# Kernel optimization log

Hardware: AMD Instinct MI355X
Metric: run time of the kernel (lower is better)

## Reference

```python
import jax, jax.numpy as jnp
import numpy as np

D_MODEL = 1024
N_HEAD = 16
HEAD_DIM = D_MODEL // N_HEAD
ROPE_BASE = 10000.0


def _weight_quant(w):
    # BitNet b1.58 ternary weight quant with per-tensor absmean scale (STE).
    scale = jnp.clip(jnp.mean(jnp.abs(w)), 1e-5, None)
    wq = jnp.clip(jnp.round(w / scale), -1.0, 1.0) * scale
    return w + jax.lax.stop_gradient(wq - w)


def _act_quant(x):
    # Per-token int8 absmax activation quant (STE).
    scale = 127.0 / jnp.clip(jnp.max(jnp.abs(x), axis=-1, keepdims=True), 1e-5, None)
    xq = jnp.clip(jnp.round(x * scale), -128.0, 127.0) / scale
    return x + jax.lax.stop_gradient(xq - x)


def _bitlinear(x, w):
    # y = act_quant(x) @ weight_quant(w).T   (torch Linear convention, no bias)
    return _act_quant(x) @ _weight_quant(w).T


def _rope(x, pos):
    # x: [B, H, T, D]; half-split rotation.
    d = x.shape[-1]
    inv_freq = 1.0 / (ROPE_BASE ** (jnp.arange(0, d, 2, dtype=jnp.float32) / d))
    ang = pos[:, None].astype(jnp.float32) * inv_freq[None, :]  # [T, D/2]
    cos, sin = jnp.cos(ang), jnp.sin(ang)
    x1, x2 = x[..., : d // 2], x[..., d // 2 :]
    return jnp.concatenate([x1 * cos - x2 * sin, x1 * sin + x2 * cos], axis=-1)


def setup_inputs() -> dict:
    key = jax.random.key(0)
    k0, k1, k2, k3, k4 = jax.random.split(key, 5)
    B, T = 2, 2048
    s = 1.0 / np.sqrt(D_MODEL)
    return {
        "x": jax.random.normal(k0, (B, T, D_MODEL), dtype=jnp.float32),
        "Wq": jax.random.normal(k1, (D_MODEL, D_MODEL), dtype=jnp.float32) * s,
        "Wk": jax.random.normal(k2, (D_MODEL, D_MODEL), dtype=jnp.float32) * s,
        "Wv": jax.random.normal(k3, (D_MODEL, D_MODEL), dtype=jnp.float32) * s,
        "Wo": jax.random.normal(k4, (D_MODEL, D_MODEL), dtype=jnp.float32) * s,
    }


def reference(x, Wq, Wk, Wv, Wo):
    B, T, C = x.shape
    pos = jnp.arange(T)
    def heads(y):
        return y.reshape(B, T, N_HEAD, HEAD_DIM).transpose(0, 2, 1, 3)  # [B,H,T,D]
    q = _rope(heads(_bitlinear(x, Wq)), pos)
    k = _rope(heads(_bitlinear(x, Wk)), pos)
    v = heads(_bitlinear(x, Wv))
    scores = jnp.einsum("bhqd,bhkd->bhqk", q, k) / jnp.sqrt(jnp.float32(HEAD_DIM))
    causal = jnp.tril(jnp.ones((T, T), dtype=bool))
    scores = jnp.where(causal[None, None], scores, jnp.finfo(scores.dtype).min)
    att = jax.nn.softmax(scores, axis=-1)
    y = jnp.einsum("bhqk,bhkd->bhqd", att, v)  # [B,H,T,D]
    y = y.transpose(0, 2, 1, 3).reshape(B, T, C)
    return _bitlinear(y, Wo)
```

## Files before the change

kernel.cpp:

```cpp
#include <hip/hip_runtime.h>
#include <hip/hip_bf16.h>
#include <math.h>

typedef __bf16 bf16_t;
typedef signed char i8_t;
typedef __attribute__((ext_vector_type(8))) __bf16 bf16x8;
typedef __attribute__((ext_vector_type(4))) __bf16 bf16x4;
typedef __attribute__((ext_vector_type(4))) float f32x4;
typedef __attribute__((ext_vector_type(4))) int i32x4;

typedef __attribute__((address_space(3))) void lds_void_t;
typedef const __attribute__((address_space(1))) void glb_void_t;
#define GLOAD_LDS(g, l) __builtin_amdgcn_global_load_lds((glb_void_t*)(g), (lds_void_t*)(l), 16, 0, 0)

#define MFMA16(a,b,c) __builtin_amdgcn_mfma_f32_16x16x32_bf16(a,b,c,0,0,0)
#define MFMAI8(a,b,c) __builtin_amdgcn_mfma_i32_16x16x64_i8(a,b,c,0,0,0)

#if __has_builtin(__builtin_amdgcn_exp2f)
#define EXP2F(x) __builtin_amdgcn_exp2f(x)
#else
#define EXP2F(x) exp2f(x)
#endif

static constexpr int TSEQ = 2048;
static constexpr int CDIM = 1024;
#define NEG_BIG (-1.0e30f)
#define Q_PRESCALE 0.18033688011112042f
#define ROPE_C 0.41524101190971284f

__global__ __launch_bounds__(256) void wreduce(const float* __restrict__ W0, const float* __restrict__ W1,
                                               const float* __restrict__ W2, const float* __restrict__ W3,
                                               double* __restrict__ partial) {
  int w = blockIdx.x >> 6, b = blockIdx.x & 63;
  const float* W = (w==0)?W0:(w==1)?W1:(w==2)?W2:W3;
  const float* base = W + (size_t)b * 16384;
  double s = 0.0;
  for (int i = threadIdx.x * 4; i < 16384; i += 1024) {
    float4 v = *(const float4*)(base + i);
    s += (double)fabsf(v.x) + (double)fabsf(v.y) + (double)fabsf(v.z) + (double)fabsf(v.w);
  }
  #pragma unroll
  for (int off = 1; off < 64; off <<= 1) s += __shfl_xor(s, off);
  __shared__ double red[4];
  if ((threadIdx.x & 63) == 0) red[threadIdx.x >> 6] = s;
  __syncthreads();
  if (threadIdx.x == 0) partial[blockIdx.x] = red[0] + red[1] + red[2] + red[3];
}

__global__ __launch_bounds__(256) void prep(const float* __restrict__ W0, const float* __restrict__ W1,
                                            const float* __restrict__ W2, const float* __restrict__ W3,
                                            const double* __restrict__ partial, float* __restrict__ wscale,
                                            i8_t* __restrict__ wq_all,
                                            const float* __restrict__ xg, i8_t* __restrict__ xqg,
                                            float* __restrict__ rowfac, float2* __restrict__ ropetab) {
  int bid = blockIdx.x;
  if (bid < 4096) {
    int w = bid >> 10;
    double ssum = 0.0;
    for (int i = 0; i < 64; ++i) ssum += partial[w * 64 + i];
    float s = fmaxf((float)(ssum * (1.0 / 1048576.0)), 1e-5f);
    if ((bid & 1023) == 0 && threadIdx.x == 0) wscale[w] = s;
    const float* W = (w==0)?W0:(w==1)?W1:(w==2)?W2:W3;
    int off = ((bid & 1023) * 256 + threadIdx.x) * 4;
    float4 v = *(const float4*)(W + off);
    char4 q;
    q.x = (i8_t)(int)fminf(fmaxf(rintf(v.x / s), -1.f), 1.f);
    q.y = (i8_t)(int)fminf(fmaxf(rintf(v.y / s), -1.f), 1.f);
    q.z = (i8_t)(int)fminf(fmaxf(rintf(v.z / s), -1.f), 1.f);
    q.w = (i8_t)(int)fminf(fmaxf(rintf(v.w / s), -1.f), 1.f);
    *(char4*)(wq_all + (size_t)w * 1048576 + off) = q;
  } else if (bid < 8192) {
    int r = bid - 4096;
    float4 v = *(const float4*)(xg + (size_t)r * 1024 + threadIdx.x * 4);
    float mx = fmaxf(fmaxf(fabsf(v.x), fabsf(v.y)), fmaxf(fabsf(v.z), fabsf(v.w)));
    #pragma unroll
    for (int off = 1; off < 64; off <<= 1) mx = fmaxf(mx, __shfl_xor(mx, off));
    __shared__ float red[4];
    if ((threadIdx.x & 63) == 0) red[threadIdx.x >> 6] = mx;
    __syncthreads();
    mx = fmaxf(fmaxf(red[0], red[1]), fmaxf(red[2], red[3]));
    mx = fmaxf(mx, 1e-5f);
    float scale = 127.0f / mx;
    if (threadIdx.x == 0) rowfac[r] = mx * (1.0f / 127.0f);
    char4 q;
    q.x = (i8_t)(int)fminf(fmaxf(rintf(v.x * scale), -128.f), 127.f);
    q.y = (i8_t)(int)fminf(fmaxf(rintf(v.y * scale), -128.f), 127.f);
    q.z = (i8_t)(int)fminf(fmaxf(rintf(v.z * scale), -128.f), 127.f);
    q.w = (i8_t)(int)fminf(fmaxf(rintf(v.w * scale), -128.f), 127.f);
    *(char4*)(xqg + (size_t)r * 1024 + threadIdx.x * 4) = q;
  } else {
    int t = (bid - 8192) * 8 + (threadIdx.x >> 5);
    int ii = threadIdx.x & 31;
    float ang = (float)t * exp2f(-(float)ii * ROPE_C);
    float sn, cs;
    sincosf(ang, &sn, &cs);
    ropetab[t * 32 + ii] = make_float2(cs, sn);
  }
}

__global__ __launch_bounds__(256) void actquant(const float* __restrict__ xg, i8_t* __restrict__ xqg,
                                                float* __restrict__ rowfac) {
  int r = blockIdx.x;
  float4 v = *(const float4*)(xg + (size_t)r * 1024 + threadIdx.x * 4);
  float mx = fmaxf(fmaxf(fabsf(v.x), fabsf(v.y)), fmaxf(fabsf(v.z), fabsf(v.w)));
  #pragma unroll
  for (int off = 1; off < 64; off <<= 1) mx = fmaxf(mx, __shfl_xor(mx, off));
  __shared__ float red[4];
  if ((threadIdx.x & 63) == 0) red[threadIdx.x >> 6] = mx;
  __syncthreads();
  mx = fmaxf(fmaxf(red[0], red[1]), fmaxf(red[2], red[3]));
  mx = fmaxf(mx, 1e-5f);
  float scale = 127.0f / mx;
  if (threadIdx.x == 0) rowfac[r] = mx * (1.0f / 127.0f);
  char4 q;
  q.x = (i8_t)(int)fminf(fmaxf(rintf(v.x * scale), -128.f), 127.f);
  q.y = (i8_t)(int)fminf(fmaxf(rintf(v.y * scale), -128.f), 127.f);
  q.z = (i8_t)(int)fminf(fmaxf(rintf(v.z * scale), -128.f), 127.f);
  q.w = (i8_t)(int)fminf(fmaxf(rintf(v.w * scale), -128.f), 127.f);
  *(char4*)(xqg + (size_t)r * 1024 + threadIdx.x * 4) = q;
}

__global__ __launch_bounds__(256) void gemm_qkv(const i8_t* __restrict__ xq, const i8_t* __restrict__ wq_all,
                                                const float* __restrict__ wscale, const float* __restrict__ rowfac,
                                                const float2* __restrict__ ropetab,
                                                bf16_t* __restrict__ qb, bf16_t* __restrict__ kb,
                                                bf16_t* __restrict__ vtb) {
  const int z = blockIdx.z;
  const i8_t* Bw = wq_all + (size_t)z * 1048576;
  const int m0 = blockIdx.x * 128, n0 = blockIdx.y * 128;
  const int tid = threadIdx.x;
  const int wave = tid >> 6, lane = tid & 63, quad = lane >> 4, l16 = lane & 15;
  const int wm = wave >> 1, wn = wave & 1;
  __shared__ __align__(16) i8_t As[128 * 64];
  __shared__ __align__(16) i8_t Bs[128 * 64];
  i32x4 zero = {0, 0, 0, 0};
  i32x4 acc[4][4];
  #pragma unroll
  for (int i = 0; i < 4; ++i)
    #pragma unroll
    for (int j = 0; j < 4; ++j) acc[i][j] = zero;

  const int row_s = tid >> 2;
  const int cg16 = (((tid & 3) - (row_s >> 1)) & 3) * 16;
  const int sw16 = ((quad + (l16 >> 1)) & 3) * 16;

  for (int kt = 0; kt < 16; ++kt) {
    __syncthreads();
    #pragma unroll
    for (int v2 = 0; v2 < 2; ++v2) {
      int v = tid + v2 * 256;
      int row = row_s + v2 * 64;
      GLOAD_LDS(&xq[(size_t)(m0 + row) * 1024 + kt * 64 + cg16], &As[v * 16]);
      GLOAD_LDS(&Bw[(size_t)(n0 + row) * 1024 + kt * 64 + cg16], &Bs[v * 16]);
    }
    __syncthreads();
    i32x4 af[4], bfr[4];
    #pragma unroll
    for (int i = 0; i < 4; ++i) af[i] = *(const i32x4*)&As[(wm * 64 + i * 16 + l16) * 64 + sw16];
    #pragma unroll
    for (int j = 0; j < 4; ++j) bfr[j] = *(const i32x4*)&Bs[(wn * 64 + j * 16 + l16) * 64 + sw16];
    if (z == 2) {
      #pragma unroll
      for (int i = 0; i < 4; ++i)
        #pragma unroll
        for (int j = 0; j < 4; ++j) acc[i][j] = MFMAI8(bfr[i], af[j], acc[i][j]);
    } else {
      #pragma unroll
      for (int i = 0; i < 4; ++i)
        #pragma unroll
        for (int j = 0; j < 4; ++j) acc[i][j] = MFMAI8(af[i], bfr[j], acc[i][j]);
    }
  }
  float ws = wscale[z] * (z == 0 ? Q_PRESCALE : 1.0f);
  if (z <= 1) {
    bf16_t* dst = (z == 0) ? qb : kb;
    const int h = (n0 >> 6) + wn;
    #pragma unroll
    for (int i = 0; i < 4; ++i) {
      #pragma unroll
      for (int r = 0; r < 4; ++r) {
        int m = m0 + wm * 64 + i * 16 + quad * 4 + r;
        float rf = rowfac[m] * ws;
        int b = m >> 11, t = m & 2047;
        bf16_t* drow = dst + (((size_t)b * 16 + h) * 2048 + t) * 64;
        #pragma unroll
        for (int j = 0; j < 2; ++j) {
          int dd1 = j * 16 + l16;
          float2 cs2 = ropetab[t * 32 + dd1];
          float v1 = (float)acc[i][j][r] * rf;
          float v2 = (float)acc[i][j + 2][r] * rf;
          drow[dd1]      = (bf16_t)(v1 * cs2.x - v2 * cs2.y);
          drow[dd1 + 32] = (bf16_t)(v1 * cs2.y + v2 * cs2.x);
        }
      }
    }
  } else {
    const int b = m0 >> 11;
    const int tbase = (m0 & 2047) + wm * 64;
    float rfj[4];
    #pragma unroll
    for (int j = 0; j < 4; ++j) rfj[j] = rowfac[m0 + wm * 64 + j * 16 + l16] * ws;
    #pragma unroll
    for (int i = 0; i < 4; ++i) {
      #pragma unroll
      for (int r = 0; r < 4; ++r) {
        int nrow = n0 + wn * 64 + i * 16 + quad * 4 + r;
        int h = nrow >> 6, dd = nrow & 63;
        bf16_t* vrow = vtb + (((size_t)b * 16 + h) * 64 + dd) * 2048 + tbase;
        #pragma unroll
        for (int j = 0; j < 4; ++j) vrow[j * 16 + l16] = (bf16_t)((float)acc[i][j][r] * rfj[j]);
      }
    }
  }
}

__global__ __launch_bounds__(256) void gemm_out(const i8_t* __restrict__ yq, const i8_t* __restrict__ wo,
                                                const float* __restrict__ wscale, const float* __restrict__ rowfac,
                                                float* __restrict__ out) {
  const int m0 = blockIdx.x * 128, n0 = blockIdx.y * 128;
  const int tid = threadIdx.x;
  const int wave = tid >> 6, lane = tid & 63, quad = lane >> 4, l16 = lane & 15;
  const int wm = wave >> 1, wn = wave & 1;
  __shared__ __align__(16) i8_t As[128 * 64];
  __shared__ __align__(16) i8_t Bs[128 * 64];
  i32x4 zero = {0, 0, 0, 0};
  i32x4 acc[4][4];
  #pragma unroll
  for (int i = 0; i < 4; ++i)
    #pragma unroll
    for (int j = 0; j < 4; ++j) acc[i][j] = zero;

  const int row_s = tid >> 2;
  const int cg16 = (((tid & 3) - (row_s >> 1)) & 3) * 16;
  const int sw16 = ((quad + (l16 >> 1)) & 3) * 16;

  for (int kt = 0; kt < 16; ++kt) {
    __syncthreads();
    #pragma unroll
    for (int v2 = 0; v2 < 2; ++v2) {
      int v = tid + v2 * 256;
      int row = row_s + v2 * 64;
      GLOAD_LDS(&yq[(size_t)(m0 + row) * 1024 + kt * 64 + cg16], &As[v * 16]);
      GLOAD_LDS(&wo[(size_t)(n0 + row) * 1024 + kt * 64 + cg16], &Bs[v * 16]);
    }
    __syncthreads();
    i32x4 af[4], bfr[4];
    #pragma unroll
    for (int i = 0; i < 4; ++i) af[i] = *(const i32x4*)&As[(wm * 64 + i * 16 + l16) * 64 + sw16];
    #pragma unroll
    for (int j = 0; j < 4; ++j) bfr[j] = *(const i32x4*)&Bs[(wn * 64 + j * 16 + l16) * 64 + sw16];
    #pragma unroll
    for (int i = 0; i < 4; ++i)
      #pragma unroll
      for (int j = 0; j < 4; ++j) acc[i][j] = MFMAI8(af[i], bfr[j], acc[i][j]);
  }
  float ws = wscale[3];
  #pragma unroll
  for (int i = 0; i < 4; ++i) {
    #pragma unroll
    for (int r = 0; r < 4; ++r) {
      int m = m0 + wm * 64 + i * 16 + quad * 4 + r;
      float rf = rowfac[m] * ws;
      #pragma unroll
      for (int j = 0; j < 4; ++j) {
        int n = n0 + wn * 64 + j * 16 + l16;
        out[(size_t)m * 1024 + n] = (float)acc[i][j][r] * rf;
      }
    }
  }
}

__global__ __launch_bounds__(512) void flash_attn(const bf16_t* __restrict__ qg, const bf16_t* __restrict__ kg,
                                                  const bf16_t* __restrict__ vtg, float* __restrict__ yf) {
  const int lid = (int)blockIdx.y * 8 + (int)blockIdx.x;
  const int p  = (lid >> 3) & 7;
  const int bh = (lid & 7) * 4 + (lid >> 6);
  const int tid = threadIdx.x;
  const int wave = tid >> 6, lane = tid & 63;
  const int quad = lane >> 4, l16 = lane & 15;

  __shared__ __align__(16) bf16_t Kb[2][64 * 64];
  __shared__ __align__(16) bf16_t Vb[2][64 * 64];
  __shared__ __align__(16) bf16_t Pl[8][16 * 72];

  const int b = bh >> 4, h = bh & 15;
  bf16_t* Pw = &Pl[wave][0];

  const int r0 = tid >> 3, cblk = tid & 7;
  const int ldsOff0 = r0 * 64 + ((cblk ^ (r0 & 7)) * 8);
  const size_t bhbase = (size_t)bh * 131072;
  const bf16_t* kbase0 = kg + bhbase + r0 * 64 + cblk * 8;
  const bf16_t* vbase0 = vtg + bhbase + r0 * 2048 + cblk * 8;

  int kf_off[4][2];
  #pragma unroll
  for (int n = 0; n < 4; ++n)
    #pragma unroll
    for (int c = 0; c < 2; ++c)
      kf_off[n][c] = (n * 16 + l16) * 64 + (((c * 4 + quad) ^ (l16 & 7)) * 8);

  bf16x8 ones;
  #pragma unroll
  for (int j = 0; j < 8; ++j) ones[j] = (bf16_t)1.0f;
  f32x4 zero = {0.f, 0.f, 0.f, 0.f};

  bf16x8 kpre = *(const bf16x8*)(kbase0);
  bf16x8 vpre = *(const bf16x8*)(vbase0);

  int cum = 0;
  #pragma unroll 1
  for (int tsel = 0; tsel < 2; ++tsel) {
    const int qt = tsel ? (15 - p) : p;
    const int kcmax = 2 * qt + 1;
    const int qbw = qt * 128 + wave * 16;

    const bf16_t* qrowp = qg + ((size_t)bh * TSEQ + qbw + l16) * 64;
    bf16x8 aq0 = *(const bf16x8*)(qrowp + quad * 8);
    bf16x8 aq1 = *(const bf16x8*)(qrowp + 32 + quad * 8);

    f32x4 o[4], o5;
    #pragma unroll
    for (int i = 0; i < 4; ++i) o[i] = zero;
    o5 = zero;

    #pragma unroll 1
    for (int kc = 0; kc <= kcmax; ++kc, ++cum) {
      const int buf = cum & 1;
      bf16_t* Kt = &Kb[buf][0];
      bf16_t* Vt = &Vb[buf][0];
      *(bf16x8*)&Kt[ldsOff0] = kpre;
      *(bf16x8*)&Vt[ldsOff0] = vpre;
      __syncthreads();
      int nkc = (kc < kcmax) ? (kc + 1) : ((tsel == 0) ? 0 : -1);
      if (nkc >= 0) {
        kpre = *(const bf16x8*)(kbase0 + nkc * 4096);
        vpre = *(const bf16x8*)(vbase0 + nkc * 64);
      }

      f32x4 s[4];
      #pragma unroll
      for (int n = 0; n < 4; ++n) {
        bf16x8 bk0 = *(const bf16x8*)&Kt[kf_off[n][0]];
        bf16x8 bk1 = *(const bf16x8*)&Kt[kf_off[n][1]];
        s[n] = MFMA16(aq1, bk1, MFMA16(aq0, bk0, zero));
      }
      if (kc * 64 + 63 > qbw) {
        #pragma unroll
        for (int n = 0; n < 4; ++n)
          #pragma unroll
          for (int r = 0; r < 4; ++r) {
            int kpos = kc * 64 + n * 16 + l16;
            int qpos = qbw + quad * 4 + r;
            if (kpos > qpos) s[n][r] = NEG_BIG;
          }
      }
      #pragma unroll
      for (int n = 0; n < 4; ++n)
        #pragma unroll
        for (int r = 0; r < 4; ++r)
          Pw[(quad * 4 + r) * 72 + n * 16 + l16] = (bf16_t)EXP2F(s[n][r]);

      bf16x8 ap0 = *(const bf16x8*)&Pw[l16 * 72 + quad * 8];
      bf16x8 ap1 = *(const bf16x8*)&Pw[l16 * 72 + 32 + quad * 8];
      #pragma unroll
      for (int nh = 0; nh < 4; ++nh) {
        bf16x8 bv0 = *(const bf16x8*)&Vt[kf_off[nh][0]];
        bf16x8 bv1 = *(const bf16x8*)&Vt[kf_off[nh][1]];
        o[nh] = MFMA16(ap1, bv1, MFMA16(ap0, bv0, o[nh]));
      }
      o5 = MFMA16(ap1, ones, MFMA16(ap0, ones, o5));
    }

    #pragma unroll
    for (int r = 0; r < 4; ++r) {
      float invl = 1.0f / o5[r];
      int t = qbw + quad * 4 + r;
      float* yrow = yf + ((size_t)b * TSEQ + t) * CDIM + h * 64;
      #pragma unroll
      for (int nh = 0; nh < 4; ++nh) yrow[nh * 16 + l16] = o[nh][r] * invl;
    }
  }
}

extern "C" void kernel_launch(void* const* d_in, const int* in_sizes, int n_in,
                              void* d_out, int out_size, void* d_ws, size_t ws_size,
                              hipStream_t stream) {
  const float* x  = (const float*)d_in[0];
  const float* Wq = (const float*)d_in[1];
  const float* Wk = (const float*)d_in[2];
  const float* Wv = (const float*)d_in[3];
  const float* Wo = (const float*)d_in[4];
  float* out = (float*)d_out;

  char* ws = (char*)d_ws;
  double* wpartial = (double*)(ws);
  float* wscale   = (float*)(ws + 4096);
  float* rowfacx  = (float*)(ws + 8192);
  float* rowfacy  = (float*)(ws + 8192 + 16384);
  i8_t* wq_all    = (i8_t*)(ws + 65536);
  i8_t* xq        = wq_all + 4194304;
  bf16_t* qb      = (bf16_t*)(xq + 4194304);
  bf16_t* kb      = qb + 4194304;
  bf16_t* vtb     = kb + 4194304;
  float*  yf      = (float*)(vtb + 4194304);
  float2* ropetab = (float2*)(yf + 4194304);
  i8_t* yq        = xq;

  wreduce<<<256, 256, 0, stream>>>(Wq, Wk, Wv, Wo, wpartial);
  prep<<<8448, 256, 0, stream>>>(Wq, Wk, Wv, Wo, wpartial, wscale, wq_all, x, xq, rowfacx, ropetab);
  gemm_qkv<<<dim3(32, 8, 3), 256, 0, stream>>>(xq, wq_all, wscale, rowfacx, ropetab, qb, kb, vtb);
  flash_attn<<<dim3(8, 32), 512, 0, stream>>>(qb, kb, vtb, yf);
  actquant<<<4096, 256, 0, stream>>>(yf, yq, rowfacy);
  gemm_out<<<dim3(32, 8), 256, 0, stream>>>(yq, wq_all + 3 * 1048576, wscale, rowfacy, out);
}
```

Measured before the change: 171.9 us.

## Halve flash-attention query tile to 64 rows with 4 waves and 512 blocks

Changes the flash attention work split from 128-query tiles handled by 8 waves to 64-query tiles handled by 4 waves, doubling the grid to 512 blocks while keeping the paired causal tile scheduling (p and 31-p). Each thread now loads two 16-byte chunks of K and V per 64-key tile, because there are half as many threads. The aim is more blocks for better CU occupancy and finer causal load balance on the MI355X. In exchange, each K/V tile is reused by fewer query rows, so global K/V traffic roughly doubles.

After: 181.8 us. +5.7%, slower.

```diff
diff --git a/kernel.cpp b/kernel.cpp
--- a/kernel.cpp
+++ b/kernel.cpp
@@ -270,27 +270,31 @@
   }
 }
 
-__global__ __launch_bounds__(512) void flash_attn(const bf16_t* __restrict__ qg, const bf16_t* __restrict__ kg,
+__global__ __launch_bounds__(256) void flash_attn(const bf16_t* __restrict__ qg, const bf16_t* __restrict__ kg,
                                                   const bf16_t* __restrict__ vtg, float* __restrict__ yf) {
   const int lid = (int)blockIdx.y * 8 + (int)blockIdx.x;
-  const int p  = (lid >> 3) & 7;
-  const int bh = (lid & 7) * 4 + (lid >> 6);
+  const int p  = (lid >> 3) & 15;
+  const int bh = (lid & 7) * 4 + (lid >> 7);
   const int tid = threadIdx.x;
   const int wave = tid >> 6, lane = tid & 63;
   const int quad = lane >> 4, l16 = lane & 15;
 
   __shared__ __align__(16) bf16_t Kb[2][64 * 64];
   __shared__ __align__(16) bf16_t Vb[2][64 * 64];
-  __shared__ __align__(16) bf16_t Pl[8][16 * 72];
+  __shared__ __align__(16) bf16_t Pl[4][16 * 72];
 
   const int b = bh >> 4, h = bh & 15;
   bf16_t* Pw = &Pl[wave][0];
 
   const int r0 = tid >> 3, cblk = tid & 7;
-  const int ldsOff0 = r0 * 64 + ((cblk ^ (r0 & 7)) * 8);
+  const int swz8 = ((cblk ^ (r0 & 7)) * 8);
+  const int ldsOffA = r0 * 64 + swz8;
+  const int ldsOffB = ldsOffA + 32 * 64;
   const size_t bhbase = (size_t)bh * 131072;
-  const bf16_t* kbase0 = kg + bhbase + r0 * 64 + cblk * 8;
-  const bf16_t* vbase0 = vtg + bhbase + r0 * 2048 + cblk * 8;
+  const bf16_t* kbaseA = kg + bhbase + r0 * 64 + cblk * 8;
+  const bf16_t* kbaseB = kbaseA + 32 * 64;
+  const bf16_t* vbaseA = vtg + bhbase + r0 * 2048 + cblk * 8;
+  const bf16_t* vbaseB = vbaseA + 32 * 2048;
 
   int kf_off[4][2];
   #pragma unroll
@@ -304,15 +308,17 @@
   for (int j = 0; j < 8; ++j) ones[j] = (bf16_t)1.0f;
   f32x4 zero = {0.f, 0.f, 0.f, 0.f};
 
-  bf16x8 kpre = *(const bf16x8*)(kbase0);
-  bf16x8 vpre = *(const bf16x8*)(vbase0);
+  bf16x8 kpreA = *(const bf16x8*)(kbaseA);
+  bf16x8 kpreB = *(const bf16x8*)(kbaseB);
+  bf16x8 vpreA = *(const bf16x8*)(vbaseA);
+  bf16x8 vpreB = *(const bf16x8*)(vbaseB);
 
   int cum = 0;
   #pragma unroll 1
   for (int tsel = 0; tsel < 2; ++tsel) {
-    const int qt = tsel ? (15 - p) : p;
-    const int kcmax = 2 * qt + 1;
-    const int qbw = qt * 128 + wave * 16;
+    const int qt = tsel ? (31 - p) : p;
+    const int kcmax = qt;
+    const int qbw = qt * 64 + wave * 16;
 
     const bf16_t* qrowp = qg + ((size_t)bh * TSEQ + qbw + l16) * 64;
     bf16x8 aq0 = *(const bf16x8*)(qrowp + quad * 8);
@@ -328,13 +334,17 @@
       const int buf = cum & 1;
       bf16_t* Kt = &Kb[buf][0];
       bf16_t* Vt = &Vb[buf][0];
-      *(bf16x8*)&Kt[ldsOff0] = kpre;
-      *(bf16x8*)&Vt[ldsOff0] = vpre;
+      *(bf16x8*)&Kt[ldsOffA] = kpreA;
+      *(bf16x8*)&Kt[ldsOffB] = kpreB;
+      *(bf16x8*)&Vt[ldsOffA] = vpreA;
+      *(bf16x8*)&Vt[ldsOffB] = vpreB;
       __syncthreads();
       int nkc = (kc < kcmax) ? (kc + 1) : ((tsel == 0) ? 0 : -1);
       if (nkc >= 0) {
-        kpre = *(const bf16x8*)(kbase0 + nkc * 4096);
-        vpre = *(const bf16x8*)(vbase0 + nkc * 64);
+        kpreA = *(const bf16x8*)(kbaseA + nkc * 4096);
+        kpreB = *(const bf16x8*)(kbaseB + nkc * 4096);
+        vpreA = *(const bf16x8*)(vbaseA + nkc * 64);
+        vpreB = *(const bf16x8*)(vbaseB + nkc * 64);
       }
 
       f32x4 s[4];
@@ -409,7 +419,7 @@
   wreduce<<<256, 256, 0, stream>>>(Wq, Wk, Wv, Wo, wpartial);
   prep<<<8448, 256, 0, stream>>>(Wq, Wk, Wv, Wo, wpartial, wscale, wq_all, x, xq, rowfacx, ropetab);
   gemm_qkv<<<dim3(32, 8, 3), 256, 0, stream>>>(xq, wq_all, wscale, rowfacx, ropetab, qb, kb, vtb);
-  flash_attn<<<dim3(8, 32), 512, 0, stream>>>(qb, kb, vtb, yf);
+  flash_attn<<<dim3(8, 64), 256, 0, stream>>>(qb, kb, vtb, yf);
   actquant<<<4096, 256, 0, stream>>>(yf, yq, rowfacy);
   gemm_out<<<dim3(32, 8), 256, 0, stream>>>(yq, wq_all + 3 * 1048576, wscale, rowfacy, out);
 }
```
